# Optimization experiments

Measured on AMD Instinct MI355X. Metric: run time of the kernel, lower is better.

Reference implementation:

```python
import jax, jax.numpy as jnp
import numpy as np

B, N, C, H, DEPTH, MLP = 8, 1024, 768, 12, 8, 3072
HD = C // H
SCALE = HD ** -0.5
EPS = 1e-5


def layer_norm(x, g, b):
    mu = jnp.mean(x, -1, keepdims=True)
    var = jnp.mean((x - mu) ** 2, -1, keepdims=True)
    return (x - mu) / jnp.sqrt(var + EPS) * g + b


def setup_inputs() -> dict:
    key = jax.random.key(0)
    ks = jax.random.split(key, 8)
    s = 0.02
    return {
        "x": jax.random.normal(ks[0], (B, N, C), jnp.float32),
        "ln1_g": jnp.ones((DEPTH, C), jnp.float32),
        "ln1_b": jnp.zeros((DEPTH, C), jnp.float32),
        "wqkv": jax.random.normal(ks[1], (DEPTH, C, 3 * C), jnp.float32) * s,
        "wproj": jax.random.normal(ks[2], (DEPTH, C, C), jnp.float32) * s,
        "bproj": jnp.zeros((DEPTH, C), jnp.float32),
        "ln2_g": jnp.ones((DEPTH, C), jnp.float32),
        "ln2_b": jnp.zeros((DEPTH, C), jnp.float32),
        "w1": jax.random.normal(ks[3], (DEPTH, C, MLP), jnp.float32) * s,
        "b1": jnp.zeros((DEPTH, MLP), jnp.float32),
        "w2": jax.random.normal(ks[4], (DEPTH, MLP, C), jnp.float32) * s,
        "b2": jnp.zeros((DEPTH, C), jnp.float32),
    }


def reference(x, ln1_g, ln1_b, wqkv, wproj, bproj, ln2_g, ln2_b, w1, b1, w2, b2):
    def body(h, p):
        g1, be1, wq, wp, bp, g2, be2, wf1, bf1, wf2, bf2 = p
        # --- attention block: Residual(PreNorm(SelfAttention)) ---
        y = layer_norm(h, g1, be1)
        qkv = (y @ wq).reshape(B, N, 3, H, HD)
        qkv = jnp.transpose(qkv, (2, 0, 3, 1, 4))  # [3, B, H, N, HD]
        q, k, v = qkv[0], qkv[1], qkv[2]
        logits = jnp.einsum("bhnd,bhmd->bhnm", q, k) * SCALE
        # source applies softmax twice (faithful to original)
        attn = jax.nn.softmax(jax.nn.softmax(logits, axis=-1), axis=-1)
        o = jnp.einsum("bhnm,bhmd->bhnd", attn, v)
        o = jnp.transpose(o, (0, 2, 1, 3)).reshape(B, N, C)
        h = h + o @ wp + bp
        # --- FFN block: Residual(PreNorm(FeedForward)) ---
        y2 = layer_norm(h, g2, be2)
        f = jax.nn.relu(y2 @ wf1 + bf1) @ wf2 + bf2
        return h + f, None

    out, _ = jax.lax.scan(body, x, (ln1_g, ln1_b, wqkv, wproj, bproj, ln2_g, ln2_b, w1, b1, w2, b2))
    return out
```

## Files before the change

### kernel.cpp

```cpp
#include <hip/hip_runtime.h>
#include <hip/hip_bf16.h>

#define DEPTHL 8
#define BZ 8
#define SEQ 1024
#define CDIM 768
#define HEADS 12
#define HDIM 64
#define MLPD 3072
#define TOK (BZ*SEQ)
#define QKVN (3*CDIM)

typedef __attribute__((ext_vector_type(8))) short vshort8;
typedef __attribute__((ext_vector_type(4))) short vshort4;
typedef __attribute__((ext_vector_type(4))) float vfloat4;

__device__ __forceinline__ short bf16_bits(float f) {
  union { float f; unsigned u; } x; x.f = f;
  unsigned r = (x.u + 0x7FFFu + ((x.u >> 16) & 1u)) >> 16;
  return (short)r;
}

__device__ __forceinline__ unsigned pk_bf16(float a, float b) {
  unsigned r;
  asm("v_cvt_pk_bf16_f32 %0, %1, %2" : "=v"(r) : "v"(a), "v"(b));
  return r;
}

#define GL16(g, l) __builtin_amdgcn_global_load_lds( \
    (const __attribute__((address_space(1))) unsigned int*)(g), \
    (__attribute__((address_space(3))) unsigned int*)(l), 16, 0, 0)

__global__ __launch_bounds__(256) void wconv_t(const float* __restrict__ in,
                                               short* __restrict__ out,
                                               int K, int N) {
  __shared__ float tile[32][33];
  const long d = blockIdx.z;
  in  += d * (long)K * N;
  out += d * (long)N * K;
  const int n0 = blockIdx.x * 32, k0 = blockIdx.y * 32;
  const int tx = threadIdx.x & 31, ty = threadIdx.x >> 5;
#pragma unroll
  for (int i = 0; i < 4; i++)
    tile[ty + 8*i][tx] = in[(long)(k0 + ty + 8*i) * N + n0 + tx];
  __syncthreads();
#pragma unroll
  for (int i = 0; i < 4; i++)
    out[(long)(n0 + ty + 8*i) * K + k0 + tx] = bf16_bits(tile[tx][ty + 8*i]);
}

__global__ __launch_bounds__(256) void vtrans(const short* __restrict__ qkv,
                                              short* __restrict__ vt) {
  __shared__ short tile[32][34];
  const int bh = blockIdx.z;
  const int b = bh / HEADS, hh = bh % HEADS;
  const int t0 = blockIdx.x * 32, d0 = blockIdx.y * 32;
  const int tx = threadIdx.x & 31, ty = threadIdx.x >> 5;
  const short* src = qkv + ((long)b * SEQ + t0) * QKVN + 2 * CDIM + hh * HDIM + d0;
#pragma unroll
  for (int i = 0; i < 4; i++)
    tile[ty + 8*i][tx] = src[(long)(ty + 8*i) * QKVN + tx];
  __syncthreads();
  short* dst = vt + (long)bh * HDIM * SEQ + (long)d0 * SEQ + t0;
#pragma unroll
  for (int i = 0; i < 4; i++)
    dst[(long)(ty + 8*i) * SEQ + tx] = tile[tx][ty + 8*i];
}

__global__ __launch_bounds__(256) void ln_fwd(const float* __restrict__ h,
                                              const float* __restrict__ g,
                                              const float* __restrict__ be,
                                              short* __restrict__ y) {
  const int row = blockIdx.x * 4 + (threadIdx.x >> 6);
  const int lane = threadIdx.x & 63;
  const float4* hr = (const float4*)(h + (long)row * CDIM);
  const float4 v0 = hr[lane], v1 = hr[lane + 64], v2 = hr[lane + 128];
  float s = (v0.x + v0.y + v0.z + v0.w) + (v1.x + v1.y + v1.z + v1.w)
          + (v2.x + v2.y + v2.z + v2.w);
#pragma unroll
  for (int m = 32; m >= 1; m >>= 1) s += __shfl_xor(s, m);
  const float mu = s * (1.0f / CDIM);
  float d0x = v0.x - mu, d0y = v0.y - mu, d0z = v0.z - mu, d0w = v0.w - mu;
  float d1x = v1.x - mu, d1y = v1.y - mu, d1z = v1.z - mu, d1w = v1.w - mu;
  float d2x = v2.x - mu, d2y = v2.y - mu, d2z = v2.z - mu, d2w = v2.w - mu;
  float q = (d0x*d0x + d0y*d0y + d0z*d0z + d0w*d0w)
          + (d1x*d1x + d1y*d1y + d1z*d1z + d1w*d1w)
          + (d2x*d2x + d2y*d2y + d2z*d2z + d2w*d2w);
#pragma unroll
  for (int m = 32; m >= 1; m >>= 1) q += __shfl_xor(q, m);
  const float rstd = rsqrtf(q * (1.0f / CDIM) + 1e-5f);
  const float4* gp = (const float4*)g;
  const float4* bp = (const float4*)be;
  short* yr = y + (long)row * CDIM;
#pragma unroll
  for (int c = 0; c < 3; c++) {
    const float4 g4 = gp[lane + c * 64];
    const float4 b4 = bp[lane + c * 64];
    float dx = (c == 0 ? d0x : c == 1 ? d1x : d2x);
    float dy = (c == 0 ? d0y : c == 1 ? d1y : d2y);
    float dz = (c == 0 ? d0z : c == 1 ? d1z : d2z);
    float dw = (c == 0 ? d0w : c == 1 ? d1w : d2w);
    vshort4 o;
    o[0] = bf16_bits(dx * rstd * g4.x + b4.x);
    o[1] = bf16_bits(dy * rstd * g4.y + b4.y);
    o[2] = bf16_bits(dz * rstd * g4.z + b4.z);
    o[3] = bf16_bits(dw * rstd * g4.w + b4.w);
    *(vshort4*)(yr + c * 256 + lane * 4) = o;
  }
}

template<int EPI>
__global__ __launch_bounds__(256) void gemm_bt(const short* __restrict__ A,
                                               const short* __restrict__ Bt,
                                               const float* __restrict__ bias,
                                               void* __restrict__ Cout,
                                               int M, int N, int K) {
  __shared__ short As[128 * 64];
  __shared__ short Bs[128 * 64];
  const int tid = threadIdx.x;
  const int wid = tid >> 6, lane = tid & 63;
  const int lg = lane >> 4, lr = lane & 15;
  const int wm = wid >> 1, wn = wid & 1;

  const int gx = gridDim.x;
  const int nwg = gx * gridDim.y;
  int flat = blockIdx.y * gx + blockIdx.x;
  flat = (flat & 7) * (nwg >> 3) + (flat >> 3);
  const long bx = flat % gx;
  const long by = flat / gx;

  vfloat4 acc[4][4];
#pragma unroll
  for (int i = 0; i < 4; i++)
#pragma unroll
    for (int j = 0; j < 4; j++) acc[i][j] = (vfloat4){0.f, 0.f, 0.f, 0.f};

  const short* Abase = A  + by * 128 * (long)K;
  const short* Bbase = Bt + bx * 128 * (long)K;

  for (int kk = 0; kk < K; kk += 64) {
    __syncthreads();
#pragma unroll
    for (int ch = 0; ch < 4; ch++) {
      const int dst = tid * 16 + ch * 4096;
      const int off = dst ^ (((dst >> 7) & 7) << 4);
      const long srow = off >> 7;
      const int scol = (off & 127) >> 1;
      GL16(Abase + srow * K + kk + scol, As + (dst >> 1));
      GL16(Bbase + srow * K + kk + scol, Bs + (dst >> 1));
    }
    __syncthreads();
#pragma unroll
    for (int kh = 0; kh < 2; kh++) {
      vshort8 a[4], b[4];
#pragma unroll
      for (int mt = 0; mt < 4; mt++) {
        const int row = wm * 64 + mt * 16 + lr;
        int byt = row * 128 + kh * 64 + lg * 16;
        byt ^= (row & 7) << 4;
        a[mt] = *(const vshort8*)((const char*)As + byt);
      }
#pragma unroll
      for (int nt = 0; nt < 4; nt++) {
        const int row = wn * 64 + nt * 16 + lr;
        int byt = row * 128 + kh * 64 + lg * 16;
        byt ^= (row & 7) << 4;
        b[nt] = *(const vshort8*)((const char*)Bs + byt);
      }
#pragma unroll
      for (int mt = 0; mt < 4; mt++)
#pragma unroll
        for (int nt = 0; nt < 4; nt++)
          acc[mt][nt] = __builtin_amdgcn_mfma_f32_16x16x32_bf16(a[mt], b[nt], acc[mt][nt], 0, 0, 0);
    }
  }

  const long row0 = by * 128 + wm * 64;
  const long col0 = bx * 128 + wn * 64;
#pragma unroll
  for (int mt = 0; mt < 4; mt++) {
#pragma unroll
    for (int nt = 0; nt < 4; nt++) {
      const long col = col0 + nt * 16 + lr;
      float bv = 0.f;
      if (EPI != 0) bv = bias[col];
#pragma unroll
      for (int r = 0; r < 4; r++) {
        const long row = row0 + mt * 16 + lg * 4 + r;
        float v = acc[mt][nt][r];
        if (EPI == 0) {
          ((short*)Cout)[row * N + col] = bf16_bits(v);
        } else if (EPI == 1) {
          v += bv; v = v > 0.f ? v : 0.f;
          ((short*)Cout)[row * N + col] = bf16_bits(v);
        } else {
          float* hp = (float*)Cout + row * N + col;
          *hp = *hp + v + bv;
        }
      }
    }
  }
}

__global__ __launch_bounds__(256, 4) void attn_fused4(const short* __restrict__ qkv,
                                                      const short* __restrict__ vt,
                                                      short* __restrict__ o) {
  __shared__ __align__(16) short P_lds[4 * 4096];
  __shared__ float redm[4][16], redz[4][16], redt[4][16];
  int flat = blockIdx.y * 64 + blockIdx.x;
  flat = (flat & 7) * (6144 >> 3) + (flat >> 3);
  const int qt = flat & 63;
  const int bh = flat >> 6;
  const int b = bh / HEADS, hh = bh % HEADS;
  const int tid = threadIdx.x, wid = tid >> 6, lane = tid & 63;
  const int lg = lane >> 4, lr = lane & 15;
  const long tokbase = (long)b * SEQ;
  const short* qbase = qkv + tokbase * QKVN + hh * HDIM;
  const short* kbase = qkv + tokbase * QKVN + CDIM + hh * HDIM;
  const short* vtb = vt + (long)bh * HDIM * SEQ;
  char* Pw = (char*)P_lds + wid * 8192;

  vshort8 qf[2];
#pragma unroll
  for (int ks = 0; ks < 2; ks++)
    qf[ks] = *(const vshort8*)(qbase + (long)(qt * 16 + lr) * QKVN + ks * 32 + lg * 8);

  vfloat4 s[16];
#pragma unroll
  for (int bb = 0; bb < 4; bb++) {
    vshort8 kf[8];
#pragma unroll
    for (int u = 0; u < 4; u++) {
      const int n0 = wid * 256 + (bb * 4 + u) * 16;
#pragma unroll
      for (int ks = 0; ks < 2; ks++)
        kf[u * 2 + ks] = *(const vshort8*)(kbase + (long)(n0 + lr) * QKVN + ks * 32 + lg * 8);
    }
#pragma unroll
    for (int u = 0; u < 4; u++) {
      vfloat4 acc = (vfloat4){0.f, 0.f, 0.f, 0.f};
      acc = __builtin_amdgcn_mfma_f32_16x16x32_bf16(kf[u * 2 + 0], qf[0], acc, 0, 0, 0);
      acc = __builtin_amdgcn_mfma_f32_16x16x32_bf16(kf[u * 2 + 1], qf[1], acc, 0, 0, 0);
      s[bb * 4 + u] = acc;
    }
  }

  float mt16[16];
#pragma unroll
  for (int i = 0; i < 16; i++)
    mt16[i] = fmaxf(fmaxf(s[i][0], s[i][1]), fmaxf(s[i][2], s[i][3]));
#pragma unroll
  for (int st = 8; st >= 1; st >>= 1)
#pragma unroll
    for (int i = 0; i < 8; i++) if (i < st) mt16[i] = fmaxf(mt16[i], mt16[i + st]);
  float m = mt16[0];
  m = fmaxf(m, __shfl_xor(m, 16));
  m = fmaxf(m, __shfl_xor(m, 32));
  if (lane < 16) redm[wid][lr] = m;
  __syncthreads();
  m = fmaxf(fmaxf(redm[0][lr], redm[1][lr]), fmaxf(redm[2][lr], redm[3][lr]));
  const float msc = m * 0.125f;

  float zt[16];
#pragma unroll
  for (int i = 0; i < 16; i++) {
    float e0 = __expf(fmaf(s[i][0], 0.125f, -msc));
    float e1 = __expf(fmaf(s[i][1], 0.125f, -msc));
    float e2 = __expf(fmaf(s[i][2], 0.125f, -msc));
    float e3 = __expf(fmaf(s[i][3], 0.125f, -msc));
    s[i][0] = e0; s[i][1] = e1; s[i][2] = e2; s[i][3] = e3;
    zt[i] = (e0 + e1) + (e2 + e3);
  }
#pragma unroll
  for (int st = 8; st >= 1; st >>= 1)
#pragma unroll
    for (int i = 0; i < 8; i++) if (i < st) zt[i] += zt[i + st];
  float z = zt[0];
  z += __shfl_xor(z, 16);
  z += __shfl_xor(z, 32);
  if (lane < 16) redz[wid][lr] = z;
  __syncthreads();
  z = (redz[0][lr] + redz[1][lr]) + (redz[2][lr] + redz[3][lr]);
  const float rz = 1.0f / z;

  float tt[16];
#pragma unroll
  for (int i = 0; i < 16; i++) {
    float p0 = __expf(s[i][0] * rz);
    float p1 = __expf(s[i][1] * rz);
    float p2 = __expf(s[i][2] * rz);
    float p3 = __expf(s[i][3] * rz);
    s[i][0] = p0; s[i][1] = p1; s[i][2] = p2; s[i][3] = p3;
    tt[i] = (p0 + p1) + (p2 + p3);
  }
#pragma unroll
  for (int st = 8; st >= 1; st >>= 1)
#pragma unroll
    for (int i = 0; i < 8; i++) if (i < st) tt[i] += tt[i + st];
  float t2 = tt[0];
  t2 += __shfl_xor(t2, 16);
  t2 += __shfl_xor(t2, 32);
  if (lane < 16) redt[wid][lr] = t2;
  __syncthreads();
  t2 = (redt[0][lr] + redt[1][lr]) + (redt[2][lr] + redt[3][lr]);
  const float rt = 1.0f / t2;

#pragma unroll
  for (int i = 0; i < 16; i++) {
    const int byt = (lr * 512 + i * 32 + lg * 8) ^ ((lr & 7) << 4);
    uint2 pk;
    pk.x = pk_bf16(s[i][0] * rt, s[i][1] * rt);
    pk.y = pk_bf16(s[i][2] * rt, s[i][3] * rt);
    *(uint2*)(Pw + byt) = pk;
  }

  vfloat4 oacc[4];
#pragma unroll
  for (int dt = 0; dt < 4; dt++) oacc[dt] = (vfloat4){0.f, 0.f, 0.f, 0.f};
#pragma unroll
  for (int j = 0; j < 8; j++) {
    const int abyt = (lr * 512 + j * 64 + lg * 16) ^ ((lr & 7) << 4);
    vshort8 af = *(const vshort8*)(Pw + abyt);
#pragma unroll
    for (int dt = 0; dt < 4; dt++) {
      vshort8 vb = *(const vshort8*)(vtb + (long)(dt * 16 + lr) * SEQ + wid * 256 + j * 32 + lg * 8);
      oacc[dt] = __builtin_amdgcn_mfma_f32_16x16x32_bf16(af, vb, oacc[dt], 0, 0, 0);
    }
  }

#pragma unroll
  for (int dt = 0; dt < 4; dt++)
#pragma unroll
    for (int r = 0; r < 4; r++)
      *(float*)(Pw + ((lg * 4 + r) * 64 + dt * 16 + lr) * 4) = oacc[dt][r];
  __syncthreads();

  const int q = tid >> 4, d0 = (tid & 15) * 4;
  float4 a0 = *(const float4*)((const char*)P_lds + 0 * 8192 + (q * 64 + d0) * 4);
  float4 a1 = *(const float4*)((const char*)P_lds + 1 * 8192 + (q * 64 + d0) * 4);
  float4 a2 = *(const float4*)((const char*)P_lds + 2 * 8192 + (q * 64 + d0) * 4);
  float4 a3 = *(const float4*)((const char*)P_lds + 3 * 8192 + (q * 64 + d0) * 4);
  float ox = (a0.x + a1.x) + (a2.x + a3.x);
  float oy = (a0.y + a1.y) + (a2.y + a3.y);
  float oz = (a0.z + a1.z) + (a2.z + a3.z);
  float ow = (a0.w + a1.w) + (a2.w + a3.w);
  uint2 ob;
  ob.x = pk_bf16(ox, oy);
  ob.y = pk_bf16(oz, ow);
  *(uint2*)(o + (tokbase + qt * 16 + q) * CDIM + hh * HDIM + d0) = ob;
}

extern "C" void kernel_launch(void* const* d_in, const int* in_sizes, int n_in,
                              void* d_out, int out_size, void* d_ws, size_t ws_size,
                              hipStream_t stream) {
  const float* x     = (const float*)d_in[0];
  const float* ln1_g = (const float*)d_in[1];
  const float* ln1_b = (const float*)d_in[2];
  const float* wqkv  = (const float*)d_in[3];
  const float* wproj = (const float*)d_in[4];
  const float* bproj = (const float*)d_in[5];
  const float* ln2_g = (const float*)d_in[6];
  const float* ln2_b = (const float*)d_in[7];
  const float* w1    = (const float*)d_in[8];
  const float* b1    = (const float*)d_in[9];
  const float* w2    = (const float*)d_in[10];
  const float* b2    = (const float*)d_in[11];
  float* h = (float*)d_out;

  char* ws = (char*)d_ws;
  short* wqkv_t  = (short*)ws; ws += (size_t)DEPTHL * QKVN * CDIM * 2;
  short* wproj_t = (short*)ws; ws += (size_t)DEPTHL * CDIM * CDIM * 2;
  short* w1_t    = (short*)ws; ws += (size_t)DEPTHL * MLPD * CDIM * 2;
  short* w2_t    = (short*)ws; ws += (size_t)DEPTHL * CDIM * MLPD * 2;
  short* ybf     = (short*)ws; ws += (size_t)TOK * CDIM * 2;
  short* qkvbf   = (short*)ws; ws += (size_t)TOK * QKVN * 2;
  short* obf     = (short*)ws; ws += (size_t)TOK * CDIM * 2;
  short* f1bf    = (short*)ws; ws += (size_t)TOK * MLPD * 2;
  short* vtb     = f1bf;

  hipMemcpyAsync(h, x, (size_t)TOK * CDIM * sizeof(float), hipMemcpyDeviceToDevice, stream);

  wconv_t<<<dim3(QKVN / 32, CDIM / 32, DEPTHL), 256, 0, stream>>>(wqkv, wqkv_t, CDIM, QKVN);
  wconv_t<<<dim3(CDIM / 32, CDIM / 32, DEPTHL), 256, 0, stream>>>(wproj, wproj_t, CDIM, CDIM);
  wconv_t<<<dim3(MLPD / 32, CDIM / 32, DEPTHL), 256, 0, stream>>>(w1, w1_t, CDIM, MLPD);
  wconv_t<<<dim3(CDIM / 32, MLPD / 32, DEPTHL), 256, 0, stream>>>(w2, w2_t, MLPD, CDIM);

  for (int l = 0; l < DEPTHL; l++) {
    ln_fwd<<<TOK / 4, 256, 0, stream>>>(h, ln1_g + l * CDIM, ln1_b + l * CDIM, ybf);
    gemm_bt<0><<<dim3(QKVN / 128, TOK / 128), 256, 0, stream>>>(
        ybf, wqkv_t + (size_t)l * QKVN * CDIM, nullptr, qkvbf, TOK, QKVN, CDIM);
    vtrans<<<dim3(SEQ / 32, HDIM / 32, BZ * HEADS), 256, 0, stream>>>(qkvbf, vtb);
    attn_fused4<<<dim3(SEQ / 16, BZ * HEADS), 256, 0, stream>>>(qkvbf, vtb, obf);
    gemm_bt<2><<<dim3(CDIM / 128, TOK / 128), 256, 0, stream>>>(
        obf, wproj_t + (size_t)l * CDIM * CDIM, bproj + l * CDIM, h, TOK, CDIM, CDIM);
    ln_fwd<<<TOK / 4, 256, 0, stream>>>(h, ln2_g + l * CDIM, ln2_b + l * CDIM, ybf);
    gemm_bt<1><<<dim3(MLPD / 128, TOK / 128), 256, 0, stream>>>(
        ybf, w1_t + (size_t)l * MLPD * CDIM, b1 + l * MLPD, f1bf, TOK, MLPD, CDIM);
    gemm_bt<2><<<dim3(CDIM / 128, TOK / 128), 256, 0, stream>>>(
        f1bf, w2_t + (size_t)l * CDIM * MLPD, b2 + l * CDIM, h, TOK, CDIM, MLPD);
  }
}
```

Before: 3.299 ms.

## Process two query tiles per attention block to reuse K and V fragments

The fused attention kernel now handles 32 queries per block, as two 16-row tiles, instead of 16. Each loaded K fragment and V^T fragment feeds MFMAs for both tiles, which halves global K/V traffic per query and halves the grid size. The cost is twice the score registers (two 16-vector accumulators), double the LDS for P, and dropping the occupancy hint of 4 from launch bounds, so register pressure or spills may lower occupancy.

```diff
diff --git a/kernel.cpp b/kernel.cpp
--- a/kernel.cpp
+++ b/kernel.cpp
@@ -202,15 +202,15 @@
   }
 }
 
-__global__ __launch_bounds__(256, 4) void attn_fused4(const short* __restrict__ qkv,
-                                                      const short* __restrict__ vt,
-                                                      short* __restrict__ o) {
-  __shared__ __align__(16) short P_lds[4 * 4096];
+__global__ __launch_bounds__(256) void attn_fused6(const short* __restrict__ qkv,
+                                                   const short* __restrict__ vt,
+                                                   short* __restrict__ o) {
+  __shared__ __align__(16) short P_lds[4 * 2 * 4096];
   __shared__ float redm[4][16], redz[4][16], redt[4][16];
-  int flat = blockIdx.y * 64 + blockIdx.x;
-  flat = (flat & 7) * (6144 >> 3) + (flat >> 3);
-  const int qt = flat & 63;
-  const int bh = flat >> 6;
+  int flat = blockIdx.y * 32 + blockIdx.x;
+  flat = (flat & 7) * (3072 >> 3) + (flat >> 3);
+  const int qt = flat & 31;
+  const int bh = flat >> 5;
   const int b = bh / HEADS, hh = bh % HEADS;
   const int tid = threadIdx.x, wid = tid >> 6, lane = tid & 63;
   const int lg = lane >> 4, lr = lane & 15;
@@ -218,14 +218,17 @@
   const short* qbase = qkv + tokbase * QKVN + hh * HDIM;
   const short* kbase = qkv + tokbase * QKVN + CDIM + hh * HDIM;
   const short* vtb = vt + (long)bh * HDIM * SEQ;
-  char* Pw = (char*)P_lds + wid * 8192;
-
-  vshort8 qf[2];
-#pragma unroll
-  for (int ks = 0; ks < 2; ks++)
-    qf[ks] = *(const vshort8*)(qbase + (long)(qt * 16 + lr) * QKVN + ks * 32 + lg * 8);
-
-  vfloat4 s[16];
+  char* Pw0 = (char*)P_lds + wid * 16384;
+  char* Pw1 = Pw0 + 8192;
+
+  vshort8 qf0[2], qf1[2];
+#pragma unroll
+  for (int ks = 0; ks < 2; ks++) {
+    qf0[ks] = *(const vshort8*)(qbase + (long)(qt * 32 + lr) * QKVN + ks * 32 + lg * 8);
+    qf1[ks] = *(const vshort8*)(qbase + (long)(qt * 32 + 16 + lr) * QKVN + ks * 32 + lg * 8);
+  }
+
+  vfloat4 s0[16], s1[16];
 #pragma unroll
   for (int bb = 0; bb < 4; bb++) {
     vshort8 kf[8];
@@ -238,116 +241,140 @@
     }
 #pragma unroll
     for (int u = 0; u < 4; u++) {
-      vfloat4 acc = (vfloat4){0.f, 0.f, 0.f, 0.f};
-      acc = __builtin_amdgcn_mfma_f32_16x16x32_bf16(kf[u * 2 + 0], qf[0], acc, 0, 0, 0);
-      acc = __builtin_amdgcn_mfma_f32_16x16x32_bf16(kf[u * 2 + 1], qf[1], acc, 0, 0, 0);
-      s[bb * 4 + u] = acc;
-    }
-  }
-
-  float mt16[16];
-#pragma unroll
-  for (int i = 0; i < 16; i++)
-    mt16[i] = fmaxf(fmaxf(s[i][0], s[i][1]), fmaxf(s[i][2], s[i][3]));
-#pragma unroll
-  for (int st = 8; st >= 1; st >>= 1)
-#pragma unroll
-    for (int i = 0; i < 8; i++) if (i < st) mt16[i] = fmaxf(mt16[i], mt16[i + st]);
-  float m = mt16[0];
-  m = fmaxf(m, __shfl_xor(m, 16));
-  m = fmaxf(m, __shfl_xor(m, 32));
-  if (lane < 16) redm[wid][lr] = m;
-  __syncthreads();
-  m = fmaxf(fmaxf(redm[0][lr], redm[1][lr]), fmaxf(redm[2][lr], redm[3][lr]));
-  const float msc = m * 0.125f;
-
-  float zt[16];
-#pragma unroll
-  for (int i = 0; i < 16; i++) {
-    float e0 = __expf(fmaf(s[i][0], 0.125f, -msc));
-    float e1 = __expf(fmaf(s[i][1], 0.125f, -msc));
-    float e2 = __expf(fmaf(s[i][2], 0.125f, -msc));
-    float e3 = __expf(fmaf(s[i][3], 0.125f, -msc));
-    s[i][0] = e0; s[i][1] = e1; s[i][2] = e2; s[i][3] = e3;
-    zt[i] = (e0 + e1) + (e2 + e3);
-  }
-#pragma unroll
-  for (int st = 8; st >= 1; st >>= 1)
-#pragma unroll
-    for (int i = 0; i < 8; i++) if (i < st) zt[i] += zt[i + st];
-  float z = zt[0];
-  z += __shfl_xor(z, 16);
-  z += __shfl_xor(z, 32);
-  if (lane < 16) redz[wid][lr] = z;
-  __syncthreads();
-  z = (redz[0][lr] + redz[1][lr]) + (redz[2][lr] + redz[3][lr]);
-  const float rz = 1.0f / z;
-
-  float tt[16];
-#pragma unroll
-  for (int i = 0; i < 16; i++) {
-    float p0 = __expf(s[i][0] * rz);
-    float p1 = __expf(s[i][1] * rz);
-    float p2 = __expf(s[i][2] * rz);
-    float p3 = __expf(s[i][3] * rz);
-    s[i][0] = p0; s[i][1] = p1; s[i][2] = p2; s[i][3] = p3;
-    tt[i] = (p0 + p1) + (p2 + p3);
-  }
-#pragma unroll
-  for (int st = 8; st >= 1; st >>= 1)
-#pragma unroll
-    for (int i = 0; i < 8; i++) if (i < st) tt[i] += tt[i + st];
-  float t2 = tt[0];
-  t2 += __shfl_xor(t2, 16);
-  t2 += __shfl_xor(t2, 32);
-  if (lane < 16) redt[wid][lr] = t2;
-  __syncthreads();
-  t2 = (redt[0][lr] + redt[1][lr]) + (redt[2][lr] + redt[3][lr]);
-  const float rt = 1.0f / t2;
+      vfloat4 a0 = (vfloat4){0.f, 0.f, 0.f, 0.f};
+      a0 = __builtin_amdgcn_mfma_f32_16x16x32_bf16(kf[u * 2 + 0], qf0[0], a0, 0, 0, 0);
+      a0 = __builtin_amdgcn_mfma_f32_16x16x32_bf16(kf[u * 2 + 1], qf0[1], a0, 0, 0, 0);
+      s0[bb * 4 + u] = a0;
+      vfloat4 a1 = (vfloat4){0.f, 0.f, 0.f, 0.f};
+      a1 = __builtin_amdgcn_mfma_f32_16x16x32_bf16(kf[u * 2 + 0], qf1[0], a1, 0, 0, 0);
+      a1 = __builtin_amdgcn_mfma_f32_16x16x32_bf16(kf[u * 2 + 1], qf1[1], a1, 0, 0, 0);
+      s1[bb * 4 + u] = a1;
+    }
+  }
+
+  float rt0, rt1;
+#define SOFTMAX_HALF(S, RT)                                                   \
+  {                                                                           \
+    float mt16[16];                                                           \
+    _Pragma("unroll")                                                         \
+    for (int i = 0; i < 16; i++)                                              \
+      mt16[i] = fmaxf(fmaxf(S[i][0], S[i][1]), fmaxf(S[i][2], S[i][3]));      \
+    _Pragma("unroll")                                                         \
+    for (int st = 8; st >= 1; st >>= 1)                                       \
+      _Pragma("unroll")                                                       \
+      for (int i = 0; i < 8; i++) if (i < st) mt16[i] = fmaxf(mt16[i], mt16[i + st]); \
+    float m = mt16[0];                                                        \
+    m = fmaxf(m, __shfl_xor(m, 16));                                          \
+    m = fmaxf(m, __shfl_xor(m, 32));                                          \
+    if (lane < 16) redm[wid][lr] = m;                                         \
+    __syncthreads();                                                          \
+    m = fmaxf(fmaxf(redm[0][lr], redm[1][lr]), fmaxf(redm[2][lr], redm[3][lr])); \
+    const float msc = m * 0.125f;                                             \
+    float zt[16];                                                             \
+    _Pragma("unroll")                                                         \
+    for (int i = 0; i < 16; i++) {                                            \
+      float e0 = __expf(fmaf(S[i][0], 0.125f, -msc));                         \
+      float e1 = __expf(fmaf(S[i][1], 0.125f, -msc));                         \
+      float e2 = __expf(fmaf(S[i][2], 0.125f, -msc));                         \
+      float e3 = __expf(fmaf(S[i][3], 0.125f, -msc));                         \
+      S[i][0] = e0; S[i][1] = e1; S[i][2] = e2; S[i][3] = e3;                 \
+      zt[i] = (e0 + e1) + (e2 + e3);                                          \
+    }                                                                         \
+    _Pragma("unroll")                                                         \
+    for (int st = 8; st >= 1; st >>= 1)                                       \
+      _Pragma("unroll")                                                       \
+      for (int i = 0; i < 8; i++) if (i < st) zt[i] += zt[i + st];            \
+    float z = zt[0];                                                          \
+    z += __shfl_xor(z, 16);                                                   \
+    z += __shfl_xor(z, 32);                                                   \
+    if (lane < 16) redz[wid][lr] = z;                                         \
+    __syncthreads();                                                          \
+    z = (redz[0][lr] + redz[1][lr]) + (redz[2][lr] + redz[3][lr]);            \
+    const float rz = 1.0f / z;                                                \
+    float tt[16];                                                             \
+    _Pragma("unroll")                                                         \
+    for (int i = 0; i < 16; i++) {                                            \
+      float p0 = __expf(S[i][0] * rz);                                        \
+      float p1 = __expf(S[i][1] * rz);                                        \
+      float p2 = __expf(S[i][2] * rz);                                        \
+      float p3 = __expf(S[i][3] * rz);                                        \
+      S[i][0] = p0; S[i][1] = p1; S[i][2] = p2; S[i][3] = p3;                 \
+      tt[i] = (p0 + p1) + (p2 + p3);                                          \
+    }                                                                         \
+    _Pragma("unroll")                                                         \
+    for (int st = 8; st >= 1; st >>= 1)                                       \
+      _Pragma("unroll")                                                       \
+      for (int i = 0; i < 8; i++) if (i < st) tt[i] += tt[i + st];            \
+    float t2 = tt[0];                                                         \
+    t2 += __shfl_xor(t2, 16);                                                 \
+    t2 += __shfl_xor(t2, 32);                                                 \
+    if (lane < 16) redt[wid][lr] = t2;                                        \
+    __syncthreads();                                                          \
+    t2 = (redt[0][lr] + redt[1][lr]) + (redt[2][lr] + redt[3][lr]);           \
+    RT = 1.0f / t2;                                                           \
+  }
+
+  SOFTMAX_HALF(s0, rt0)
+  SOFTMAX_HALF(s1, rt1)
+#undef SOFTMAX_HALF
 
 #pragma unroll
   for (int i = 0; i < 16; i++) {
     const int byt = (lr * 512 + i * 32 + lg * 8) ^ ((lr & 7) << 4);
-    uint2 pk;
-    pk.x = pk_bf16(s[i][0] * rt, s[i][1] * rt);
-    pk.y = pk_bf16(s[i][2] * rt, s[i][3] * rt);
-    *(uint2*)(Pw + byt) = pk;
-  }
-
-  vfloat4 oacc[4];
-#pragma unroll
-  for (int dt = 0; dt < 4; dt++) oacc[dt] = (vfloat4){0.f, 0.f, 0.f, 0.f};
+    uint2 pk0, pk1;
+    pk0.x = pk_bf16(s0[i][0] * rt0, s0[i][1] * rt0);
+    pk0.y = pk_bf16(s0[i][2] * rt0, s0[i][3] * rt0);
+    pk1.x = pk_bf16(s1[i][0] * rt1, s1[i][1] * rt1);
+    pk1.y = pk_bf16(s1[i][2] * rt1, s1[i][3] * rt1);
+    *(uint2*)(Pw0 + byt) = pk0;
+    *(uint2*)(Pw1 + byt) = pk1;
+  }
+
+  vfloat4 o0[4], o1[4];
+#pragma unroll
+  for (int dt = 0; dt < 4; dt++) {
+    o0[dt] = (vfloat4){0.f, 0.f, 0.f, 0.f};
+    o1[dt] = (vfloat4){0.f, 0.f, 0.f, 0.f};
+  }
 #pragma unroll
   for (int j = 0; j < 8; j++) {
     const int abyt = (lr * 512 + j * 64 + lg * 16) ^ ((lr & 7) << 4);
-    vshort8 af = *(const vshort8*)(Pw + abyt);
+    vshort8 af0 = *(const vshort8*)(Pw0 + abyt);
+    vshort8 af1 = *(const vshort8*)(Pw1 + abyt);
 #pragma unroll
     for (int dt = 0; dt < 4; dt++) {
       vshort8 vb = *(const vshort8*)(vtb + (long)(dt * 16 + lr) * SEQ + wid * 256 + j * 32 + lg * 8);
-      oacc[dt] = __builtin_amdgcn_mfma_f32_16x16x32_bf16(af, vb, oacc[dt], 0, 0, 0);
+      o0[dt] = __builtin_amdgcn_mfma_f32_16x16x32_bf16(af0, vb, o0[dt], 0, 0, 0);
+      o1[dt] = __builtin_amdgcn_mfma_f32_16x16x32_bf16(af1, vb, o1[dt], 0, 0, 0);
     }
   }
 
 #pragma unroll
   for (int dt = 0; dt < 4; dt++)
 #pragma unroll
-    for (int r = 0; r < 4; r++)
-      *(float*)(Pw + ((lg * 4 + r) * 64 + dt * 16 + lr) * 4) = oacc[dt][r];
+    for (int r = 0; r < 4; r++) {
+      *(float*)(Pw0 + ((lg * 4 + r) * 64 + dt * 16 + lr) * 4) = o0[dt][r];
+      *(float*)(Pw1 + ((lg * 4 + r) * 64 + dt * 16 + lr) * 4) = o1[dt][r];
+    }
   __syncthreads();
 
   const int q = tid >> 4, d0 = (tid & 15) * 4;
-  float4 a0 = *(const float4*)((const char*)P_lds + 0 * 8192 + (q * 64 + d0) * 4);
-  float4 a1 = *(const float4*)((const char*)P_lds + 1 * 8192 + (q * 64 + d0) * 4);
-  float4 a2 = *(const float4*)((const char*)P_lds + 2 * 8192 + (q * 64 + d0) * 4);
-  float4 a3 = *(const float4*)((const char*)P_lds + 3 * 8192 + (q * 64 + d0) * 4);
-  float ox = (a0.x + a1.x) + (a2.x + a3.x);
-  float oy = (a0.y + a1.y) + (a2.y + a3.y);
-  float oz = (a0.z + a1.z) + (a2.z + a3.z);
-  float ow = (a0.w + a1.w) + (a2.w + a3.w);
-  uint2 ob;
-  ob.x = pk_bf16(ox, oy);
-  ob.y = pk_bf16(oz, ow);
-  *(uint2*)(o + (tokbase + qt * 16 + q) * CDIM + hh * HDIM + d0) = ob;
+#pragma unroll
+  for (int h = 0; h < 2; h++) {
+    const int ro = h * 8192 + (q * 64 + d0) * 4;
+    float4 a0 = *(const float4*)((const char*)P_lds + 0 * 16384 + ro);
+    float4 a1 = *(const float4*)((const char*)P_lds + 1 * 16384 + ro);
+    float4 a2 = *(const float4*)((const char*)P_lds + 2 * 16384 + ro);
+    float4 a3 = *(const float4*)((const char*)P_lds + 3 * 16384 + ro);
+    float ox = (a0.x + a1.x) + (a2.x + a3.x);
+    float oy = (a0.y + a1.y) + (a2.y + a3.y);
+    float oz = (a0.z + a1.z) + (a2.z + a3.z);
+    float ow = (a0.w + a1.w) + (a2.w + a3.w);
+    uint2 ob;
+    ob.x = pk_bf16(ox, oy);
+    ob.y = pk_bf16(oz, ow);
+    *(uint2*)(o + (tokbase + qt * 32 + h * 16 + q) * CDIM + hh * HDIM + d0) = ob;
+  }
 }
 
 extern "C" void kernel_launch(void* const* d_in, const int* in_sizes, int n_in,
@@ -390,7 +417,7 @@
     gemm_bt<0><<<dim3(QKVN / 128, TOK / 128), 256, 0, stream>>>(
         ybf, wqkv_t + (size_t)l * QKVN * CDIM, nullptr, qkvbf, TOK, QKVN, CDIM);
     vtrans<<<dim3(SEQ / 32, HDIM / 32, BZ * HEADS), 256, 0, stream>>>(qkvbf, vtb);
-    attn_fused4<<<dim3(SEQ / 16, BZ * HEADS), 256, 0, stream>>>(qkvbf, vtb, obf);
+    attn_fused6<<<dim3(SEQ / 32, BZ * HEADS), 256, 0, stream>>>(qkvbf, vtb, obf);
     gemm_bt<2><<<dim3(CDIM / 128, TOK / 128), 256, 0, stream>>>(
         obf, wproj_t + (size_t)l * CDIM * CDIM, bproj + l * CDIM, h, TOK, CDIM, CDIM);
     ln_fwd<<<TOK / 4, 256, 0, stream>>>(h, ln2_g + l * CDIM, ln2_b + l * CDIM, ybf);
```

After: 3.310 ms (median of 2 runs). About the same (+0.3%).
